# Optimization experiments

Hardware: AMD Instinct MI355X
Metric: run time of the kernel (lower is better)

## Reference

```python
import jax, jax.numpy as jnp
import numpy as np

N_NODES = 100000
N_EDGES = 3200000
N_GRAPHS = 16
C = 64            # sage_channels
L = 6             # sage_layers
H = 32            # linear_channels
EPS = 1e-5

def layer_norm(x, g, b):
    mu = jnp.mean(x, axis=-1, keepdims=True)
    var = jnp.mean((x - mu) ** 2, axis=-1, keepdims=True)
    return (x - mu) * jax.lax.rsqrt(var + EPS) * g + b

def setup_inputs() -> dict:
    key = jax.random.key(0)
    ks = jax.random.split(key, 24)
    s = 1.0 / np.sqrt(C)
    inp = {
        'x': jax.random.normal(ks[0], (N_NODES, C), dtype=jnp.float32),
        'edge_index': jax.random.randint(ks[1], (2, N_EDGES), 0, N_NODES, dtype=jnp.int64),
        'batch': jnp.sort(jax.random.randint(ks[2], (N_NODES,), 0, N_GRAPHS, dtype=jnp.int64)),
        # 6 SAGE layers, each: lin_l (W+b) on aggregated, lin_r (W, no bias) on root, LayerNorm (g,b)
        'sage_Wl': jax.random.uniform(ks[3], (L, C, C), jnp.float32, -s, s),
        'sage_bl': jax.random.uniform(ks[4], (L, C), jnp.float32, -s, s),
        'sage_Wr': jax.random.uniform(ks[5], (L, C, C), jnp.float32, -s, s),
        'sage_g': jnp.ones((L, C), jnp.float32),
        'sage_b': jnp.zeros((L, C), jnp.float32),
        'mlp0_W': jax.random.uniform(ks[6], (C, H), jnp.float32, -s, s),
        'mlp0_b': jax.random.uniform(ks[7], (H,), jnp.float32, -s, s),
        'mlp0_g': jnp.ones((H,), jnp.float32),
        'mlp0_bn': jnp.zeros((H,), jnp.float32),
        'mlp_W': jax.random.uniform(ks[8], (3, H, H), jnp.float32, -1/np.sqrt(H), 1/np.sqrt(H)),
        'mlp_b': jax.random.uniform(ks[9], (3, H), jnp.float32, -1/np.sqrt(H), 1/np.sqrt(H)),
        'mlp_g': jnp.ones((3, H), jnp.float32),
        'mlp_bn': jnp.zeros((3, H), jnp.float32),
        'head_W': jax.random.uniform(ks[10], (H, 1), jnp.float32, -1/np.sqrt(H), 1/np.sqrt(H)),
        'head_b': jax.random.uniform(ks[11], (1,), jnp.float32, -1/np.sqrt(H), 1/np.sqrt(H)),
    }
    return inp

def reference(x, edge_index, batch, sage_Wl, sage_bl, sage_Wr, sage_g, sage_b,
              mlp0_W, mlp0_b, mlp0_g, mlp0_bn, mlp_W, mlp_b, mlp_g, mlp_bn, head_W, head_b):
    src, dst = edge_index[0], edge_index[1]
    # in-degree for mean aggregation (messages flow src -> dst), clamp to 1
    deg = jax.ops.segment_sum(jnp.ones((src.shape[0],), x.dtype), dst, num_segments=N_NODES)
    inv_deg = (1.0 / jnp.maximum(deg, 1.0))[:, None]
    h = x
    for i in range(L):
        msg_sum = jax.ops.segment_sum(h[src], dst, num_segments=N_NODES)  # [N, C]
        agg = msg_sum * inv_deg
        f = agg @ sage_Wl[i] + sage_bl[i] + h @ sage_Wr[i]
        f = jax.nn.gelu(f, approximate=False)
        f = layer_norm(f, sage_g[i], sage_b[i])
        h = f + h  # residual (all 6 appended blocks have with_residual=True)
    pooled = jax.ops.segment_max(h, batch, num_segments=N_GRAPHS)  # [G, C]
    z = layer_norm(jax.nn.gelu(pooled @ mlp0_W + mlp0_b, approximate=False), mlp0_g, mlp0_bn)
    for i in range(3):
        t = layer_norm(jax.nn.gelu(z @ mlp_W[i] + mlp_b[i], approximate=False), mlp_g[i], mlp_bn[i])
        z = t + z
    return z @ head_W + head_b  # [G, 1]
```

## Files before the change

### kernel.cpp

```cpp
#include <hip/hip_runtime.h>
#include <hip/hip_bf16.h>
#include <math.h>

#define N_NODES 100000
#define N_EDGES 3200000
#define N_GRAPHS 16
#define C 64
#define L 6
#define H 32
#define EPS 1e-5f

static const int SCAN_BLOCKS = (N_NODES + 1023) / 1024;

__device__ __forceinline__ float gelu_exact(float x) {
    return 0.5f * x * (1.0f + erff(x * 0.70710678118654752440f));
}

__device__ __forceinline__ float wave_sum64(float v) {
#pragma unroll
    for (int m = 32; m >= 1; m >>= 1) v += __shfl_xor(v, m, 64);
    return v;
}

__device__ __forceinline__ float sum32(float v) {
#pragma unroll
    for (int m = 16; m >= 1; m >>= 1) v += __shfl_xor(v, m, 64);
    return v;
}

__device__ __forceinline__ unsigned short f32_to_bf16_rne(float f) {
    unsigned int u = __float_as_uint(f);
    u = (u + 0x7FFFu + ((u >> 16) & 1u)) >> 16;
    return (unsigned short)u;
}

#define ACC4(acc, u)                                      \
    {                                                     \
        acc.x += __uint_as_float((u).x << 16);            \
        acc.y += __uint_as_float((u).x & 0xFFFF0000u);    \
        acc.z += __uint_as_float((u).y << 16);            \
        acc.w += __uint_as_float((u).y & 0xFFFF0000u);    \
    }


__global__ void k_count(const int* __restrict__ dst, int* __restrict__ degc,
                        int* __restrict__ epos) {
    int i = blockIdx.x * blockDim.x + threadIdx.x;
    int stride = gridDim.x * blockDim.x;
    for (int e = i; e < N_EDGES; e += stride) {
        int pos = __hip_atomic_fetch_add(&degc[dst[e]], 1, __ATOMIC_RELAXED,
                                         __HIP_MEMORY_SCOPE_AGENT);
        epos[e] = pos;
    }
}

__global__ __launch_bounds__(256) void k_scan1(const int* __restrict__ degc,
                                               int* __restrict__ scanned,
                                               int* __restrict__ bsum) {
    __shared__ int sc[2][256];
    int tid = threadIdx.x;
    int base = blockIdx.x * 1024 + tid * 4;
    int c0 = (base + 0 < N_NODES) ? degc[base + 0] : 0;
    int c1 = (base + 1 < N_NODES) ? degc[base + 1] : 0;
    int c2 = (base + 2 < N_NODES) ? degc[base + 2] : 0;
    int c3 = (base + 3 < N_NODES) ? degc[base + 3] : 0;
    int p0 = c0, p1 = p0 + c1, p2 = p1 + c2, p3 = p2 + c3;
    sc[0][tid] = p3;
    __syncthreads();
    int pb = 0;
    for (int offd = 1; offd < 256; offd <<= 1) {
        int v = sc[pb][tid];
        if (tid >= offd) v += sc[pb][tid - offd];
        sc[pb ^ 1][tid] = v;
        __syncthreads();
        pb ^= 1;
    }
    int incl = sc[pb][tid];
    int exth = incl - p3;
    if (base + 0 < N_NODES) scanned[base + 0] = exth + p0;
    if (base + 1 < N_NODES) scanned[base + 1] = exth + p1;
    if (base + 2 < N_NODES) scanned[base + 2] = exth + p2;
    if (base + 3 < N_NODES) scanned[base + 3] = exth + p3;
    if (tid == 255) bsum[blockIdx.x] = incl;
}

__global__ void k_scan2(const int* __restrict__ bsum, int* __restrict__ boff,
                        int* __restrict__ rowst) {
    int run = 0;
    for (int b = 0; b < SCAN_BLOCKS; ++b) { boff[b] = run; run += bsum[b]; }
    rowst[N_NODES] = run;
}

__global__ void k_scan3(const int* __restrict__ degc, const int* __restrict__ scanned,
                        const int* __restrict__ boff, int* __restrict__ rowst) {
    int i = blockIdx.x * blockDim.x + threadIdx.x;
    if (i < N_NODES) rowst[i] = boff[i >> 10] + scanned[i] - degc[i];
}

__global__ void k_fill(const int* __restrict__ src, const int* __restrict__ dst,
                       const int* __restrict__ rowst, const int* __restrict__ epos,
                       int* __restrict__ esrc) {
    int i = blockIdx.x * blockDim.x + threadIdx.x;
    int stride = gridDim.x * blockDim.x;
    for (int e = i; e < N_EDGES; e += stride) {
        int d = dst[e];
        esrc[rowst[d] + epos[e]] = src[e];
    }
}

__global__ void k_cvt(const float* __restrict__ x, unsigned short* __restrict__ hbf) {
    int i = blockIdx.x * blockDim.x + threadIdx.x;
    int stride = gridDim.x * blockDim.x;
    for (int k = i; k < N_NODES * C / 4; k += stride) {
        float4 v = ((const float4*)x)[k];
        ushort4 o;
        o.x = f32_to_bf16_rne(v.x);
        o.y = f32_to_bf16_rne(v.y);
        o.z = f32_to_bf16_rne(v.z);
        o.w = f32_to_bf16_rne(v.w);
        ((ushort4*)hbf)[k] = o;
    }
}


__global__ __launch_bounds__(256) void k_agg(const unsigned short* __restrict__ hbf,
                                             const int* __restrict__ rowst,
                                             const int* __restrict__ esrc,
                                             float* __restrict__ agg) {
    const uint2* __restrict__ hb2 = (const uint2*)hbf;
    int wave = threadIdx.x >> 6, lane = threadIdx.x & 63;
    int n = blockIdx.x * 4 + wave;
    if (n >= N_NODES) return;
    int s0 = rowst[n], s1 = rowst[n + 1];
    int esub = lane >> 4;
    int cq = lane & 15;
    float4 accA = make_float4(0.f, 0.f, 0.f, 0.f);
    float4 accB = make_float4(0.f, 0.f, 0.f, 0.f);
    int j = s0;
    for (; j + 16 <= s1; j += 16) {
        int sA = esrc[j + 0 + esub];
        int sB = esrc[j + 4 + esub];
        int sC = esrc[j + 8 + esub];
        int sD = esrc[j + 12 + esub];
        uint2 a = hb2[sA * 16 + cq];
        uint2 b = hb2[sB * 16 + cq];
        uint2 c = hb2[sC * 16 + cq];
        uint2 d = hb2[sD * 16 + cq];
        ACC4(accA, a);
        ACC4(accB, b);
        ACC4(accA, c);
        ACC4(accB, d);
    }
    for (; j + 4 <= s1; j += 4) {
        int s = esrc[j + esub];
        uint2 a = hb2[s * 16 + cq];
        ACC4(accA, a);
    }
    if (j < s1) {
        int jj = j + esub;
        bool v = jj < s1;
        int s = v ? esrc[jj] : 0;
        uint2 a = hb2[s * 16 + cq];
        if (!v) { a.x = 0; a.y = 0; }
        ACC4(accB, a);
    }
    accA.x += accB.x; accA.y += accB.y; accA.z += accB.z; accA.w += accB.w;
#pragma unroll
    for (int m = 16; m <= 32; m <<= 1) {
        accA.x += __shfl_xor(accA.x, m, 64);
        accA.y += __shfl_xor(accA.y, m, 64);
        accA.z += __shfl_xor(accA.z, m, 64);
        accA.w += __shfl_xor(accA.w, m, 64);
    }
    int cnt = s1 - s0;
    float inv = 1.0f / (float)max(cnt, 1);
    if (lane < 16) {
        float4 r = make_float4(accA.x * inv, accA.y * inv, accA.z * inv, accA.w * inv);
        ((float4*)agg)[(size_t)n * 16 + lane] = r;
    }
}


__global__ __launch_bounds__(256) void k_sage(const float* __restrict__ h,
                                              const float* __restrict__ agg,
                                              const float* __restrict__ Wl,
                                              const float* __restrict__ bl,
                                              const float* __restrict__ Wr,
                                              const float* __restrict__ gn,
                                              const float* __restrict__ bn,
                                              float* __restrict__ hout,
                                              unsigned short* __restrict__ hbf) {
    __shared__ float rowA[4][C];
    __shared__ float rowH[4][C];
    int lane = threadIdx.x & 63;
    int wave = threadIdx.x >> 6;
    float wl[C], wr[C];
#pragma unroll
    for (int j = 0; j < C; ++j) wl[j] = Wl[j * C + lane];
#pragma unroll
    for (int j = 0; j < C; ++j) wr[j] = Wr[j * C + lane];
    float blc = bl[lane], gc = gn[lane], bc = bn[lane];

    const float4* a4 = (const float4*)rowA[wave];
    const float4* h4s = (const float4*)rowH[wave];
    for (int n = blockIdx.x * 4 + wave; n < N_NODES; n += 2048 * 4) {
        float av = agg[(size_t)n * C + lane];
        float hv = h[(size_t)n * C + lane];
        rowA[wave][lane] = av;
        rowH[wave][lane] = hv;
        float acc = blc;
#pragma unroll
        for (int k4 = 0; k4 < C / 4; ++k4) {
            float4 a = a4[k4];
            float4 b = h4s[k4];
            acc += a.x * wl[4 * k4 + 0] + a.y * wl[4 * k4 + 1] +
                   a.z * wl[4 * k4 + 2] + a.w * wl[4 * k4 + 3];
            acc += b.x * wr[4 * k4 + 0] + b.y * wr[4 * k4 + 1] +
                   b.z * wr[4 * k4 + 2] + b.w * wr[4 * k4 + 3];
        }
        float f = gelu_exact(acc);
        float mu = wave_sum64(f) * (1.0f / C);
        float d = f - mu;
        float var = wave_sum64(d * d) * (1.0f / C);
        float y = d * rsqrtf(var + EPS) * gc + bc;
        float res = y + hv;
        hout[(size_t)n * C + lane] = res;
        hbf[(size_t)n * C + lane] = f32_to_bf16_rne(res);
    }
}


__global__ __launch_bounds__(256) void k_pool_partial(const float* __restrict__ h,
                                                      const int* __restrict__ batch,
                                                      float* __restrict__ partial) {
    __shared__ float pp[4][N_GRAPHS][C];
    int lane = threadIdx.x & 63, wave = threadIdx.x >> 6;
#pragma unroll
    for (int g = 0; g < N_GRAPHS; ++g) pp[wave][g][lane] = -INFINITY;
    int chunk = (N_NODES + gridDim.x - 1) / gridDim.x;
    int start = blockIdx.x * chunk;
    int end = min(start + chunk, N_NODES);
    for (int n = start + wave; n < end; n += 4) {
        int g = batch[n];
        float v = h[(size_t)n * C + lane];
        pp[wave][g][lane] = fmaxf(pp[wave][g][lane], v);
    }
    __syncthreads();
    for (int g = wave * 4; g < wave * 4 + 4; ++g) {
        float m = fmaxf(fmaxf(pp[0][g][lane], pp[1][g][lane]),
                        fmaxf(pp[2][g][lane], pp[3][g][lane]));
        partial[(size_t)blockIdx.x * (N_GRAPHS * C) + g * C + lane] = m;
    }
}

__global__ void k_pool_final(const float* __restrict__ partial, float* __restrict__ pooled) {
    int t = threadIdx.x;
    float m = -INFINITY;
    for (int b = 0; b < 128; ++b) m = fmaxf(m, partial[b * (N_GRAPHS * C) + t]);
    pooled[t] = m;
}


__global__ __launch_bounds__(512) void k_head(const float* __restrict__ pooled,
                                              const float* __restrict__ W0,
                                              const float* __restrict__ b0,
                                              const float* __restrict__ g0,
                                              const float* __restrict__ bn0,
                                              const float* __restrict__ W,
                                              const float* __restrict__ bb,
                                              const float* __restrict__ gg,
                                              const float* __restrict__ bnn,
                                              const float* __restrict__ hW,
                                              const float* __restrict__ hb,
                                              float* __restrict__ out) {
    __shared__ float ps[N_GRAPHS][C];
    __shared__ float zs[N_GRAPHS][H];
    int t = threadIdx.x;
    for (int i = t; i < N_GRAPHS * C; i += 512) ps[i >> 6][i & 63] = pooled[i];
    __syncthreads();
    int g = t >> 5, j = t & 31;
    float acc = b0[j];
#pragma unroll 8
    for (int k = 0; k < C; ++k) acc += ps[g][k] * W0[k * H + j];
    acc = gelu_exact(acc);
    float mu = sum32(acc) * (1.0f / H);
    float d = acc - mu;
    float var = sum32(d * d) * (1.0f / H);
    float z = d * rsqrtf(var + EPS) * g0[j] + bn0[j];
    zs[g][j] = z;
    __syncthreads();
    for (int i = 0; i < 3; ++i) {
        float a = bb[i * H + j];
#pragma unroll 8
        for (int k = 0; k < H; ++k) a += zs[g][k] * W[i * H * H + k * H + j];
        a = gelu_exact(a);
        float mu2 = sum32(a) * (1.0f / H);
        float d2 = a - mu2;
        float v2 = sum32(d2 * d2) * (1.0f / H);
        float tt = d2 * rsqrtf(v2 + EPS) * gg[i * H + j] + bnn[i * H + j];
        float zn = tt + zs[g][j];
        __syncthreads();
        zs[g][j] = zn;
        __syncthreads();
    }
    float hv = zs[g][j] * hW[j];
    hv = sum32(hv);
    if (j == 0) out[g] = hv + hb[0];
}


extern "C" void kernel_launch(void* const* d_in, const int* in_sizes, int n_in,
                              void* d_out, int out_size, void* d_ws, size_t ws_size,
                              hipStream_t stream) {
    const float* x    = (const float*)d_in[0];
    const int* edge   = (const int*)d_in[1];
    const int* batch  = (const int*)d_in[2];
    const float* sWl  = (const float*)d_in[3];
    const float* sbl  = (const float*)d_in[4];
    const float* sWr  = (const float*)d_in[5];
    const float* sg   = (const float*)d_in[6];
    const float* sb   = (const float*)d_in[7];
    const float* W0   = (const float*)d_in[8];
    const float* b0   = (const float*)d_in[9];
    const float* g0   = (const float*)d_in[10];
    const float* bn0  = (const float*)d_in[11];
    const float* mW   = (const float*)d_in[12];
    const float* mb   = (const float*)d_in[13];
    const float* mg   = (const float*)d_in[14];
    const float* mbn  = (const float*)d_in[15];
    const float* hW   = (const float*)d_in[16];
    const float* hb   = (const float*)d_in[17];
    float* out = (float*)d_out;

    const int* esrc_in = edge;
    const int* edst_in = edge + N_EDGES;

    char* ws = (char*)d_ws;
    size_t off = 0;
    auto alloc = [&](size_t bytes) {
        void* p = ws + off;
        off = (off + bytes + 1023) & ~(size_t)1023;
        return p;
    };
    float* h      = (float*)alloc((size_t)N_NODES * C * 4);
    float* agg    = (float*)alloc((size_t)N_NODES * C * 4);
    unsigned short* hbf = (unsigned short*)alloc((size_t)N_NODES * C * 2);
    int* degc     = (int*)alloc((size_t)N_NODES * 4);
    int* scanned  = (int*)alloc((size_t)N_NODES * 4);
    int* rowst    = (int*)alloc((size_t)(N_NODES + 1) * 4);
    int* esrc     = (int*)alloc((size_t)N_EDGES * 4);
    int* epos     = (int*)alloc((size_t)N_EDGES * 4);
    int* bsum     = (int*)alloc(128 * 4);
    int* boff     = (int*)alloc(128 * 4);
    float* part   = (float*)alloc((size_t)128 * N_GRAPHS * C * 4);
    float* pooled = (float*)alloc((size_t)N_GRAPHS * C * 4);
    (void)ws_size;

    hipMemsetAsync(degc, 0, (size_t)N_NODES * 4, stream);
    hipMemcpyAsync(h, x, (size_t)N_NODES * C * 4, hipMemcpyDeviceToDevice, stream);

    k_count<<<2048, 256, 0, stream>>>(edst_in, degc, epos);
    k_cvt<<<1600, 256, 0, stream>>>(x, hbf);
    k_scan1<<<SCAN_BLOCKS, 256, 0, stream>>>(degc, scanned, bsum);
    k_scan2<<<1, 1, 0, stream>>>(bsum, boff, rowst);
    k_scan3<<<(N_NODES + 255) / 256, 256, 0, stream>>>(degc, scanned, boff, rowst);
    k_fill<<<2048, 256, 0, stream>>>(esrc_in, edst_in, rowst, epos, esrc);

    for (int i = 0; i < L; ++i) {
        k_agg<<<N_NODES / 4, 256, 0, stream>>>(hbf, rowst, esrc, agg);
        k_sage<<<2048, 256, 0, stream>>>(h, agg, sWl + (size_t)i * C * C, sbl + (size_t)i * C,
                                         sWr + (size_t)i * C * C, sg + (size_t)i * C,
                                         sb + (size_t)i * C, h, hbf);
    }

    k_pool_partial<<<128, 256, 0, stream>>>(h, batch, part);
    k_pool_final<<<1, 1024, 0, stream>>>(part, pooled);
    k_head<<<1, 512, 0, stream>>>(pooled, W0, b0, g0, bn0, mW, mb, mg, mbn, hW, hb, out);
}
```

Baseline: 1.254 ms.

## Partially sort CSR neighbors by source range and drop initial h copy

Edges are bucketed per destination into four source-index ranges, so each node's neighbor list is roughly grouped by source region. The aim is better cache locality in the gather during aggregation. The first SAGE layer also reads x directly, which removes the device-to-device copy of x into h. In exchange, the count and scan arrays grow fourfold and the count and fill kernels each do an extra division.

```diff
diff --git a/kernel.cpp b/kernel.cpp
--- a/kernel.cpp
+++ b/kernel.cpp
@@ -9,8 +9,11 @@
 #define L 6
 #define H 32
 #define EPS 1e-5f
-
-static const int SCAN_BLOCKS = (N_NODES + 1023) / 1024;
+#define NPARTS 4
+#define PART_DIV 25000
+#define NBUCKETS (N_NODES * NPARTS)
+
+static const int SCAN_BLOCKS = (NBUCKETS + 1023) / 1024;
 
 __device__ __forceinline__ float gelu_exact(float x) {
     return 0.5f * x * (1.0f + erff(x * 0.70710678118654752440f));
@@ -43,13 +46,14 @@
     }
 
 
-__global__ void k_count(const int* __restrict__ dst, int* __restrict__ degc,
-                        int* __restrict__ epos) {
+__global__ void k_count(const int* __restrict__ src, const int* __restrict__ dst,
+                        int* __restrict__ degc, int* __restrict__ epos) {
     int i = blockIdx.x * blockDim.x + threadIdx.x;
     int stride = gridDim.x * blockDim.x;
     for (int e = i; e < N_EDGES; e += stride) {
-        int pos = __hip_atomic_fetch_add(&degc[dst[e]], 1, __ATOMIC_RELAXED,
-                                         __HIP_MEMORY_SCOPE_AGENT);
+        int part = src[e] / PART_DIV;
+        int pos = __hip_atomic_fetch_add(&degc[dst[e] * NPARTS + part], 1,
+                                         __ATOMIC_RELAXED, __HIP_MEMORY_SCOPE_AGENT);
         epos[e] = pos;
     }
 }
@@ -60,10 +64,10 @@
     __shared__ int sc[2][256];
     int tid = threadIdx.x;
     int base = blockIdx.x * 1024 + tid * 4;
-    int c0 = (base + 0 < N_NODES) ? degc[base + 0] : 0;
-    int c1 = (base + 1 < N_NODES) ? degc[base + 1] : 0;
-    int c2 = (base + 2 < N_NODES) ? degc[base + 2] : 0;
-    int c3 = (base + 3 < N_NODES) ? degc[base + 3] : 0;
+    int c0 = (base + 0 < NBUCKETS) ? degc[base + 0] : 0;
+    int c1 = (base + 1 < NBUCKETS) ? degc[base + 1] : 0;
+    int c2 = (base + 2 < NBUCKETS) ? degc[base + 2] : 0;
+    int c3 = (base + 3 < NBUCKETS) ? degc[base + 3] : 0;
     int p0 = c0, p1 = p0 + c1, p2 = p1 + c2, p3 = p2 + c3;
     sc[0][tid] = p3;
     __syncthreads();
@@ -77,10 +81,10 @@
     }
     int incl = sc[pb][tid];
     int exth = incl - p3;
-    if (base + 0 < N_NODES) scanned[base + 0] = exth + p0;
-    if (base + 1 < N_NODES) scanned[base + 1] = exth + p1;
-    if (base + 2 < N_NODES) scanned[base + 2] = exth + p2;
-    if (base + 3 < N_NODES) scanned[base + 3] = exth + p3;
+    if (base + 0 < NBUCKETS) scanned[base + 0] = exth + p0;
+    if (base + 1 < NBUCKETS) scanned[base + 1] = exth + p1;
+    if (base + 2 < NBUCKETS) scanned[base + 2] = exth + p2;
+    if (base + 3 < NBUCKETS) scanned[base + 3] = exth + p3;
     if (tid == 255) bsum[blockIdx.x] = incl;
 }
 
@@ -88,13 +92,13 @@
                         int* __restrict__ rowst) {
     int run = 0;
     for (int b = 0; b < SCAN_BLOCKS; ++b) { boff[b] = run; run += bsum[b]; }
-    rowst[N_NODES] = run;
+    rowst[NBUCKETS] = run;
 }
 
 __global__ void k_scan3(const int* __restrict__ degc, const int* __restrict__ scanned,
                         const int* __restrict__ boff, int* __restrict__ rowst) {
     int i = blockIdx.x * blockDim.x + threadIdx.x;
-    if (i < N_NODES) rowst[i] = boff[i >> 10] + scanned[i] - degc[i];
+    if (i < NBUCKETS) rowst[i] = boff[i >> 10] + scanned[i] - degc[i];
 }
 
 __global__ void k_fill(const int* __restrict__ src, const int* __restrict__ dst,
@@ -103,8 +107,9 @@
     int i = blockIdx.x * blockDim.x + threadIdx.x;
     int stride = gridDim.x * blockDim.x;
     for (int e = i; e < N_EDGES; e += stride) {
-        int d = dst[e];
-        esrc[rowst[d] + epos[e]] = src[e];
+        int s = src[e];
+        int part = s / PART_DIV;
+        esrc[rowst[dst[e] * NPARTS + part] + epos[e]] = s;
     }
 }
 
@@ -131,7 +136,7 @@
     int wave = threadIdx.x >> 6, lane = threadIdx.x & 63;
     int n = blockIdx.x * 4 + wave;
     if (n >= N_NODES) return;
-    int s0 = rowst[n], s1 = rowst[n + 1];
+    int s0 = rowst[n * NPARTS], s1 = rowst[n * NPARTS + NPARTS];
     int esub = lane >> 4;
     int cq = lane & 15;
     float4 accA = make_float4(0.f, 0.f, 0.f, 0.f);
@@ -345,30 +350,30 @@
     float* h      = (float*)alloc((size_t)N_NODES * C * 4);
     float* agg    = (float*)alloc((size_t)N_NODES * C * 4);
     unsigned short* hbf = (unsigned short*)alloc((size_t)N_NODES * C * 2);
-    int* degc     = (int*)alloc((size_t)N_NODES * 4);
-    int* scanned  = (int*)alloc((size_t)N_NODES * 4);
-    int* rowst    = (int*)alloc((size_t)(N_NODES + 1) * 4);
+    int* degc     = (int*)alloc((size_t)NBUCKETS * 4);
+    int* scanned  = (int*)alloc((size_t)NBUCKETS * 4);
+    int* rowst    = (int*)alloc((size_t)(NBUCKETS + 1) * 4);
     int* esrc     = (int*)alloc((size_t)N_EDGES * 4);
     int* epos     = (int*)alloc((size_t)N_EDGES * 4);
-    int* bsum     = (int*)alloc(128 * 4);
-    int* boff     = (int*)alloc(128 * 4);
+    int* bsum     = (int*)alloc(512 * 4);
+    int* boff     = (int*)alloc(512 * 4);
     float* part   = (float*)alloc((size_t)128 * N_GRAPHS * C * 4);
     float* pooled = (float*)alloc((size_t)N_GRAPHS * C * 4);
     (void)ws_size;
 
-    hipMemsetAsync(degc, 0, (size_t)N_NODES * 4, stream);
-    hipMemcpyAsync(h, x, (size_t)N_NODES * C * 4, hipMemcpyDeviceToDevice, stream);
-
-    k_count<<<2048, 256, 0, stream>>>(edst_in, degc, epos);
+    hipMemsetAsync(degc, 0, (size_t)NBUCKETS * 4, stream);
+
+    k_count<<<2048, 256, 0, stream>>>(esrc_in, edst_in, degc, epos);
     k_cvt<<<1600, 256, 0, stream>>>(x, hbf);
     k_scan1<<<SCAN_BLOCKS, 256, 0, stream>>>(degc, scanned, bsum);
     k_scan2<<<1, 1, 0, stream>>>(bsum, boff, rowst);
-    k_scan3<<<(N_NODES + 255) / 256, 256, 0, stream>>>(degc, scanned, boff, rowst);
+    k_scan3<<<(NBUCKETS + 255) / 256, 256, 0, stream>>>(degc, scanned, boff, rowst);
     k_fill<<<2048, 256, 0, stream>>>(esrc_in, edst_in, rowst, epos, esrc);
 
     for (int i = 0; i < L; ++i) {
         k_agg<<<N_NODES / 4, 256, 0, stream>>>(hbf, rowst, esrc, agg);
-        k_sage<<<2048, 256, 0, stream>>>(h, agg, sWl + (size_t)i * C * C, sbl + (size_t)i * C,
+        k_sage<<<2048, 256, 0, stream>>>(i == 0 ? x : h, agg,
+                                         sWl + (size_t)i * C * C, sbl + (size_t)i * C,
                                          sWr + (size_t)i * C * C, sg + (size_t)i * C,
                                          sb + (size_t)i * C, h, hbf);
     }
```

After: 1.231 ms. No clear change (-1.8%).
